# Kernel tuning notes

Measured on AMD Instinct MI355X. Metric: run time of the kernel, lower is better.

## Reference

```python
import jax, jax.numpy as jnp
import numpy as np

HID = 256
DT = 0.05
B = 131072


def setup_inputs() -> dict:
    key = jax.random.key(0)
    ks = jax.random.split(key, 20)
    n = jax.random.normal
    inp = {
        "q": n(ks[0], (B, 1), jnp.float32),
        "p": n(ks[1], (B, 1), jnp.float32),
        "u": n(ks[2], (B, 1), jnp.float32),
        # kinetic MLP T(q_enc, p): in dim 3
        "kW1": n(ks[3], (HID, 3), jnp.float32) / np.sqrt(3.0),
        "kb1": n(ks[4], (HID,), jnp.float32) * 0.01,
        "kW2": n(ks[5], (HID, HID), jnp.float32) / np.sqrt(HID),
        "kb2": n(ks[6], (HID,), jnp.float32) * 0.01,
        "kW3": n(ks[7], (1, HID), jnp.float32) / np.sqrt(HID),
        "kb3": n(ks[8], (1,), jnp.float32) * 0.01,
        # potential MLP V(q_enc): in dim 2
        "pW1": n(ks[9], (HID, 2), jnp.float32) / np.sqrt(2.0),
        "pb1": n(ks[10], (HID,), jnp.float32) * 0.01,
        "pW2": n(ks[11], (HID, HID), jnp.float32) / np.sqrt(HID),
        "pb2": n(ks[12], (HID,), jnp.float32) * 0.01,
        "pW3": n(ks[13], (1, HID), jnp.float32) / np.sqrt(HID),
        "pb3": n(ks[14], (1,), jnp.float32) * 0.01,
        # learned structure matrices (std=0.01 as in nn.init.normal_)
        "A": n(ks[15], (2, 2), jnp.float32) * 0.01,
        "L_param": n(ks[16], (2, 2), jnp.float32) * 0.01,
        "b_ctrl": n(ks[17], (1, 1), jnp.float32) * 0.01,
    }
    return inp


def reference(q, p, u, kW1, kb1, kW2, kb2, kW3, kb3,
              pW1, pb1, pW2, pb2, pW3, pb3, A, L_param, b_ctrl):
    sp = jax.nn.softplus

    def H_sum(z):  # z: [B,2] -> scalar sum of H over batch
        q_, p_ = z[:, :1], z[:, 1:]
        enc = jnp.concatenate([jnp.sin(q_), jnp.cos(q_)], axis=-1)  # [B,2]
        x = jnp.concatenate([enc, p_], axis=-1)                      # [B,3]
        h = sp(x @ kW1.T + kb1)
        h = sp(h @ kW2.T + kb2)
        T = (h @ kW3.T + kb3)[:, 0]
        g = sp(enc @ pW1.T + pb1)
        g = sp(g @ pW2.T + pb2)
        V = (g @ pW3.T + pb3)[:, 0]
        return jnp.sum(T + V)

    # M = J - R with J = A - A^T, R = L L^T, L = strict-lower + softplus(diag)
    J = A - A.T
    L = jnp.tril(L_param, -1) + jnp.diag(sp(jnp.diagonal(L_param)))
    M = J - L @ L.T                          # [2,2]
    Bu = u @ b_ctrl.T                        # [B,1]
    zeros_q = jnp.zeros_like(q)

    def dyn(q_, p_):
        # torch detaches z before autograd.grad -> stop_gradient here
        z = jax.lax.stop_gradient(jnp.concatenate([q_, p_], axis=-1))
        gH = jax.grad(H_sum)(z)              # [B,2] = dH/dz per sample
        dz = gH @ M.T + jnp.concatenate([zeros_q, Bu], axis=-1)
        return dz[:, :1], dz[:, 1:]

    dt = DT
    dq1, dp1 = dyn(q, p)
    dq2, dp2 = dyn(q + 0.5 * dt * dq1, p + 0.5 * dt * dp1)
    dq3, dp3 = dyn(q + 0.5 * dt * dq2, p + 0.5 * dt * dp2)
    dq4, dp4 = dyn(q + dt * dq3, p + dt * dp3)
    q_next = q + dt / 6.0 * (dq1 + 2 * dq2 + 2 * dq3 + dq4)
    p_next = p + dt / 6.0 * (dp1 + 2 * dp2 + 2 * dp3 + dp4)
    return jnp.concatenate([q_next, p_next], axis=-1)  # [B,2]
```

## Files before the change

kernel.cpp:

```cpp
#include <hip/hip_runtime.h>

#define HID 256
#define BT 64
#define DTC 0.05f

typedef __attribute__((ext_vector_type(4))) float f32x4;
typedef __attribute__((ext_vector_type(8))) __bf16 bf16x8;

__device__ __forceinline__ unsigned cvt_pk_bf16(float lo, float hi) {
    unsigned r;
    asm("v_cvt_pk_bf16_f32 %0, %1, %2" : "=v"(r) : "v"(lo), "v"(hi));
    return r;
}

__device__ __forceinline__ unsigned short f2bf(float f) {
    unsigned int x = __float_as_uint(f);
    x += 0x7fffu + ((x >> 16) & 1u);
    return (unsigned short)(x >> 16);
}
__device__ __forceinline__ float bf2f(unsigned short s) {
    return __uint_as_float(((unsigned int)s) << 16);
}

#define OFF_FWDT 0
#define OFF_BWDT 65536
#define OFF_FWDV 131072
#define OFF_BWDV 196608
#define OFF_PROJT 262144
#define OFF_PROJV 266240
#define TOTAL_PRE 270336

__global__ void prepack_kernel(const float* __restrict__ kW1, const float* __restrict__ kW2,
                               const float* __restrict__ pW1, const float* __restrict__ pW2,
                               unsigned short* __restrict__ ws) {
    int t = blockIdx.x * 256 + threadIdx.x;
    if (t >= TOTAL_PRE) return;
    float v;
    if (t < OFF_FWDV) {
        int tt = t & 65535;
        bool bwd = t >= OFF_BWDT;
        int j = tt & 7, lane = (tt >> 3) & 63, kk = (tt >> 9) & 7, nt = tt >> 12;
        int n = nt * 16 + (lane & 15);
        int k = kk * 32 + (lane >> 4) * 8 + j;
        v = bwd ? kW2[k * HID + n] : kW2[n * HID + k];
    } else if (t < OFF_PROJT) {
        int tt = (t - OFF_FWDV) & 65535;
        bool bwd = t >= OFF_BWDV;
        int j = tt & 7, lane = (tt >> 3) & 63, kk = (tt >> 9) & 7, nt = tt >> 12;
        int n = nt * 16 + (lane & 15);
        int k = kk * 32 + (lane >> 4) * 8 + j;
        v = bwd ? pW2[k * HID + n] : pW2[n * HID + k];
    } else if (t < OFF_PROJV) {
        int tt = t - OFF_PROJT;
        int j = tt & 7, lane = (tt >> 3) & 63, kk = tt >> 9;
        int c = lane & 15;
        int k = kk * 32 + (lane >> 4) * 8 + j;
        v = (c < 3) ? kW1[k * 3 + c] : 0.f;
    } else {
        int tt = t - OFF_PROJV;
        int j = tt & 7, lane = (tt >> 3) & 63, kk = tt >> 9;
        int c = lane & 15;
        int k = kk * 32 + (lane >> 4) * 8 + j;
        v = (c < 2) ? pW1[k * 2 + c] : 0.f;
    }
    ws[t] = f2bf(v);
}


#define MFMA __builtin_amdgcn_mfma_f32_16x16x32_bf16

template <int IND, int NOUT>
__device__ __forceinline__ void run_net(
    char* bufAc, char* bufBc,
    const float* sh_sin, const float* sh_cos, const float* sh_pv,
    const float* __restrict__ W1, const float* __restrict__ b1g,
    const float* __restrict__ b2g, const float* __restrict__ W3,
    const unsigned short* __restrict__ fwdB, const unsigned short* __restrict__ bwdB,
    const unsigned short* __restrict__ projB,
    float* g0, float* g1, float* g2,
    int w, int lane)
{
    const int lr = lane & 15;
    const int lg = lane >> 4;
    const unsigned int arx = (unsigned)(lr & 7) << 4;
    const unsigned int cbase = ((unsigned)lg << 4) ^ arx;

    {
        float w0[2], w1v[2], w2v[2], b1v[2];
#pragma unroll
        for (int nt = 0; nt < 2; ++nt) {
            int j = w * 32 + nt * 16 + lr;
            w0[nt]  = W1[j * IND + 0];
            w1v[nt] = W1[j * IND + 1];
            w2v[nt] = (IND == 3) ? W1[j * IND + 2] : 0.f;
            b1v[nt] = b1g[j];
        }
#pragma unroll
        for (int mt = 0; mt < 4; ++mt) {
#pragma unroll
            for (int r = 0; r < 4; ++r) {
                int row = mt * 16 + lg * 4 + r;
                float sv = sh_sin[row], cv = sh_cos[row];
                float pv = (IND == 3) ? sh_pv[row] : 0.f;
                unsigned int rowx = (unsigned)(row & 7) << 4;
                char* rowp = bufAc + row * 512;
                float sp[2];
#pragma unroll
                for (int nt = 0; nt < 2; ++nt) {
                    float x = fmaf(w0[nt], sv, b1v[nt]);
                    x = fmaf(w1v[nt], cv, x);
                    if (IND == 3) x = fmaf(w2v[nt], pv, x);
                    float e = __expf(-fabsf(x));
                    sp[nt] = fmaxf(x, 0.f) + __logf(1.f + e);
                }
                unsigned d01 = cvt_pk_bf16(sp[0], sp[1]);
                int j0 = w * 32 + lr;
                *(unsigned short*)(rowp + (((j0 +  0) * 2) ^ rowx)) = (unsigned short)d01;
                *(unsigned short*)(rowp + (((j0 + 16) * 2) ^ rowx)) = (unsigned short)(d01 >> 16);
            }
        }
    }
    __syncthreads();

    f32x4 acc[4][2];
#pragma unroll
    for (int mt = 0; mt < 4; ++mt)
#pragma unroll
        for (int nt = 0; nt < 2; ++nt)
            acc[mt][nt] = (f32x4){0.f, 0.f, 0.f, 0.f};
    {
        const unsigned short* fb = fwdB + (w * 2) * 8 * 512 + lane * 8;
#pragma unroll 1
        for (int kk = 0; kk < 8; ++kk) {
            bf16x8 bv0 = *(const bf16x8*)(fb + (0 * 8 + kk) * 512);
            bf16x8 bv1 = *(const bf16x8*)(fb + (1 * 8 + kk) * 512);
            unsigned int off = cbase ^ (unsigned)(kk << 6);
#pragma unroll
            for (int mt = 0; mt < 4; ++mt) {
                bf16x8 af = *(const bf16x8*)(bufAc + (mt * 16 + lr) * 512 + off);
                acc[mt][0] = MFMA(af, bv0, acc[mt][0], 0, 0, 0);
                acc[mt][1] = MFMA(af, bv1, acc[mt][1], 0, 0, 0);
            }
        }
    }

    {
        float b2v[2], w3v[2];
#pragma unroll
        for (int nt = 0; nt < 2; ++nt) {
            int j = w * 32 + nt * 16 + lr;
            b2v[nt] = b2g[j];
            w3v[nt] = W3[j];
        }
#pragma unroll
        for (int nt = 0; nt < 2; ++nt) {
            int i = w * 32 + nt * 16 + lr;
#pragma unroll
            for (int mt = 0; mt < 4; ++mt) {
                float val[4];
#pragma unroll
                for (int r = 0; r < 4; ++r) {
                    float x = acc[mt][nt][r] + b2v[nt];
                    float e = __expf(-fabsf(x));
                    float t = __builtin_amdgcn_rcpf(1.f + e);
                    float sg = (x < 0.f) ? e * t : t;
                    val[r] = w3v[nt] * sg;
                }
                unsigned d01 = cvt_pk_bf16(val[0], val[1]);
                unsigned d23 = cvt_pk_bf16(val[2], val[3]);
#pragma unroll
                for (int r = 0; r < 4; ++r) {
                    int row = mt * 16 + lg * 4 + r;
                    unsigned short hv = (r == 0) ? (unsigned short)d01
                                      : (r == 1) ? (unsigned short)(d01 >> 16)
                                      : (r == 2) ? (unsigned short)d23
                                                 : (unsigned short)(d23 >> 16);
                    *(unsigned short*)(bufBc + row * 512 + ((i * 2) ^ ((unsigned)(row & 7) << 4))) = hv;
                }
            }
        }
    }
    __syncthreads();

#pragma unroll
    for (int mt = 0; mt < 4; ++mt)
#pragma unroll
        for (int nt = 0; nt < 2; ++nt)
            acc[mt][nt] = (f32x4){0.f, 0.f, 0.f, 0.f};
    {
        const unsigned short* bb = bwdB + (w * 2) * 8 * 512 + lane * 8;
#pragma unroll 1
        for (int kk = 0; kk < 8; ++kk) {
            bf16x8 bv0 = *(const bf16x8*)(bb + (0 * 8 + kk) * 512);
            bf16x8 bv1 = *(const bf16x8*)(bb + (1 * 8 + kk) * 512);
            unsigned int off = cbase ^ (unsigned)(kk << 6);
#pragma unroll
            for (int mt = 0; mt < 4; ++mt) {
                bf16x8 af = *(const bf16x8*)(bufBc + (mt * 16 + lr) * 512 + off);
                acc[mt][0] = MFMA(af, bv0, acc[mt][0], 0, 0, 0);
                acc[mt][1] = MFMA(af, bv1, acc[mt][1], 0, 0, 0);
            }
        }
    }

#pragma unroll
    for (int mt = 0; mt < 4; ++mt) {
#pragma unroll
        for (int r = 0; r < 4; ++r) {
            int row = mt * 16 + lg * 4 + r;
            unsigned int rowx = (unsigned)(row & 7) << 4;
            char* rowp = bufAc + row * 512;
            int j0 = w * 32 + lr;
            unsigned short* a0 = (unsigned short*)(rowp + (((j0 +  0) * 2) ^ rowx));
            unsigned short* a1 = (unsigned short*)(rowp + (((j0 + 16) * 2) ^ rowx));
            float sg0 = 1.f - __expf(-bf2f(*a0));
            float sg1 = 1.f - __expf(-bf2f(*a1));
            unsigned d01 = cvt_pk_bf16(acc[mt][0][r] * sg0, acc[mt][1][r] * sg1);
            *a0 = (unsigned short)d01;
            *a1 = (unsigned short)(d01 >> 16);
        }
    }
    __syncthreads();

    if (w < 4) {
        const unsigned short* pb = projB + lane * 8;
        f32x4 pacc = (f32x4){0.f, 0.f, 0.f, 0.f};
        char* arow = bufAc + (w * 16 + lr) * 512;
#pragma unroll 1
        for (int kk = 0; kk < 8; ++kk) {
            bf16x8 bv = *(const bf16x8*)(pb + kk * 512);
            bf16x8 af = *(const bf16x8*)(arow + (cbase ^ (unsigned)(kk << 6)));
            pacc = MFMA(af, bv, pacc, 0, 0, 0);
        }
        if (lr < NOUT) {
            float* dst = (lr == 0) ? g0 : ((lr == 1) ? g1 : g2);
#pragma unroll
            for (int r = 0; r < 4; ++r) dst[w * 16 + lg * 4 + r] = pacc[r];
        }
    }
    __syncthreads();
}

__global__ __launch_bounds__(512, 2) void phgn_kernel(
    const float* __restrict__ q, const float* __restrict__ p, const float* __restrict__ u,
    const float* __restrict__ kW1, const float* __restrict__ kb1,
    const float* __restrict__ kb2, const float* __restrict__ kW3,
    const float* __restrict__ pW1, const float* __restrict__ pb1,
    const float* __restrict__ pb2, const float* __restrict__ pW3,
    const float* __restrict__ A, const float* __restrict__ Lp, const float* __restrict__ bctrl,
    const unsigned short* __restrict__ ws, float* __restrict__ out)
{
    __shared__ __attribute__((aligned(16))) unsigned short bufA[BT * HID];
    __shared__ __attribute__((aligned(16))) unsigned short bufB[BT * HID];
    __shared__ float sh_sin[BT], sh_cos[BT], sh_pv[BT];
    __shared__ float gx0[BT], gx1[BT], gx2[BT], ge0[BT], ge1[BT];

    const int tid = threadIdx.x;
    const int w = tid >> 6, lane = tid & 63;
    const int base = blockIdx.x * BT;

    float l00 = __logf(1.f + __expf(Lp[0]));
    float l11 = __logf(1.f + __expf(Lp[3]));
    float l10 = Lp[2];
    float J01 = A[1] - A[2];
    float M00 = -(l00 * l00);
    float M01 = J01 - l00 * l10;
    float M10 = -J01 - l10 * l00;
    float M11 = -(l10 * l10 + l11 * l11);

    float q0 = 0.f, p0 = 0.f, buv = 0.f, aq = 0.f, ap = 0.f;
    if (tid < BT) {
        q0 = q[base + tid]; p0 = p[base + tid]; buv = u[base + tid] * bctrl[0];
        float s, c; __sincosf(q0, &s, &c);
        sh_sin[tid] = s; sh_cos[tid] = c; sh_pv[tid] = p0;
    }
    __syncthreads();

    char* bufAc = (char*)bufA;
    char* bufBc = (char*)bufB;
#pragma unroll 1
    for (int s = 0; s < 4; ++s) {
        run_net<3, 3>(bufAc, bufBc, sh_sin, sh_cos, sh_pv, kW1, kb1, kb2, kW3,
                      ws + OFF_FWDT, ws + OFF_BWDT, ws + OFF_PROJT, gx0, gx1, gx2, w, lane);
        run_net<2, 2>(bufAc, bufBc, sh_sin, sh_cos, sh_pv, pW1, pb1, pb2, pW3,
                      ws + OFF_FWDV, ws + OFF_BWDV, ws + OFF_PROJV, ge0, ge1, ge1, w, lane);
        if (tid < BT) {
            float gq = (gx0[tid] + ge0[tid]) * sh_cos[tid] - (gx1[tid] + ge1[tid]) * sh_sin[tid];
            float gp = gx2[tid];
            float dq = M00 * gq + M01 * gp;
            float dp = M10 * gq + M11 * gp + buv;
            float wgt = (s == 0 || s == 3) ? 1.f : 2.f;
            aq += wgt * dq; ap += wgt * dp;
            if (s < 3) {
                float cs = (s == 2) ? 1.f : 0.5f;
                float qs = fmaf(cs * DTC, dq, q0);
                float ps = fmaf(cs * DTC, dp, p0);
                float sn, cn; __sincosf(qs, &sn, &cn);
                sh_sin[tid] = sn; sh_cos[tid] = cn; sh_pv[tid] = ps;
            } else {
                float qn = fmaf(DTC / 6.f, aq, q0);
                float pn = fmaf(DTC / 6.f, ap, p0);
                ((float2*)out)[base + tid] = make_float2(qn, pn);
            }
        }
        __syncthreads();
    }
}

extern "C" void kernel_launch(void* const* d_in, const int* in_sizes, int n_in,
                              void* d_out, int out_size, void* d_ws, size_t ws_size,
                              hipStream_t stream) {
    const float* q    = (const float*)d_in[0];
    const float* p    = (const float*)d_in[1];
    const float* u    = (const float*)d_in[2];
    const float* kW1  = (const float*)d_in[3];
    const float* kb1  = (const float*)d_in[4];
    const float* kW2  = (const float*)d_in[5];
    const float* kb2  = (const float*)d_in[6];
    const float* kW3  = (const float*)d_in[7];
    const float* pW1  = (const float*)d_in[9];
    const float* pb1  = (const float*)d_in[10];
    const float* pW2  = (const float*)d_in[11];
    const float* pb2  = (const float*)d_in[12];
    const float* pW3  = (const float*)d_in[13];
    const float* A    = (const float*)d_in[15];
    const float* Lp   = (const float*)d_in[16];
    const float* bctl = (const float*)d_in[17];
    unsigned short* ws = (unsigned short*)d_ws;
    float* out = (float*)d_out;
    int B = in_sizes[0];

    prepack_kernel<<<(TOTAL_PRE + 255) / 256, 256, 0, stream>>>(kW1, kW2, pW1, pW2, ws);
    phgn_kernel<<<B / BT, 512, 0, stream>>>(q, p, u, kW1, kb1, kb2, kW3,
                                            pW1, pb1, pb2, pW3, A, Lp, bctl, ws, out);
}
```

Before: 756.3 us.

## Hoist per-thread weights, prefetch B fragments, keep layer-1 sigmoid in registers

Per-thread first-layer weights, biases and output weights for both MLPs are loaded once per kernel into registers instead of on every RK stage. Global B-fragment loads are software-pipelined one k-step ahead, and the first fragments are issued before the barrier to hide latency. The layer-1 sigmoid derivative is computed exactly at forward time and kept packed in registers as bf16, replacing the LDS reread and exp-based reconstruction in the backward pass. The M coefficients are made wave-uniform via readfirstlane. These changes raise register pressure, which could hurt occupancy under the 512x2 launch bounds.

```diff
diff --git a/kernel.cpp b/kernel.cpp
--- a/kernel.cpp
+++ b/kernel.cpp
@@ -18,8 +18,9 @@
     x += 0x7fffu + ((x >> 16) & 1u);
     return (unsigned short)(x >> 16);
 }
-__device__ __forceinline__ float bf2f(unsigned short s) {
-    return __uint_as_float(((unsigned int)s) << 16);
+
+__device__ __forceinline__ float sgpr_f(float v) {
+    return __uint_as_float(__builtin_amdgcn_readfirstlane(__float_as_uint(v)));
 }
 
 #define OFF_FWDT 0
@@ -69,12 +70,13 @@
 
 #define MFMA __builtin_amdgcn_mfma_f32_16x16x32_bf16
 
+struct NetRegs { float w0[2], w1[2], w2[2], b1[2], b2[2], w3[2]; };
+
 template <int IND, int NOUT>
 __device__ __forceinline__ void run_net(
     char* bufAc, char* bufBc,
     const float* sh_sin, const float* sh_cos, const float* sh_pv,
-    const float* __restrict__ W1, const float* __restrict__ b1g,
-    const float* __restrict__ b2g, const float* __restrict__ W3,
+    const NetRegs& R,
     const unsigned short* __restrict__ fwdB, const unsigned short* __restrict__ bwdB,
     const unsigned short* __restrict__ projB,
     float* g0, float* g1, float* g2,
@@ -85,41 +87,39 @@
     const unsigned int arx = (unsigned)(lr & 7) << 4;
     const unsigned int cbase = ((unsigned)lg << 4) ^ arx;
 
-    {
-        float w0[2], w1v[2], w2v[2], b1v[2];
-#pragma unroll
-        for (int nt = 0; nt < 2; ++nt) {
-            int j = w * 32 + nt * 16 + lr;
-            w0[nt]  = W1[j * IND + 0];
-            w1v[nt] = W1[j * IND + 1];
-            w2v[nt] = (IND == 3) ? W1[j * IND + 2] : 0.f;
-            b1v[nt] = b1g[j];
-        }
-#pragma unroll
-        for (int mt = 0; mt < 4; ++mt) {
-#pragma unroll
-            for (int r = 0; r < 4; ++r) {
-                int row = mt * 16 + lg * 4 + r;
-                float sv = sh_sin[row], cv = sh_cos[row];
-                float pv = (IND == 3) ? sh_pv[row] : 0.f;
-                unsigned int rowx = (unsigned)(row & 7) << 4;
-                char* rowp = bufAc + row * 512;
-                float sp[2];
-#pragma unroll
-                for (int nt = 0; nt < 2; ++nt) {
-                    float x = fmaf(w0[nt], sv, b1v[nt]);
-                    x = fmaf(w1v[nt], cv, x);
-                    if (IND == 3) x = fmaf(w2v[nt], pv, x);
-                    float e = __expf(-fabsf(x));
-                    sp[nt] = fmaxf(x, 0.f) + __logf(1.f + e);
-                }
-                unsigned d01 = cvt_pk_bf16(sp[0], sp[1]);
-                int j0 = w * 32 + lr;
-                *(unsigned short*)(rowp + (((j0 +  0) * 2) ^ rowx)) = (unsigned short)d01;
-                *(unsigned short*)(rowp + (((j0 + 16) * 2) ^ rowx)) = (unsigned short)(d01 >> 16);
-            }
-        }
-    }
+    unsigned s1p[16];
+
+#pragma unroll
+    for (int mt = 0; mt < 4; ++mt) {
+#pragma unroll
+        for (int r = 0; r < 4; ++r) {
+            int row = mt * 16 + lg * 4 + r;
+            float sv = sh_sin[row], cv = sh_cos[row];
+            float pv = (IND == 3) ? sh_pv[row] : 0.f;
+            unsigned int rowx = (unsigned)(row & 7) << 4;
+            char* rowp = bufAc + row * 512;
+            float sp[2], sg[2];
+#pragma unroll
+            for (int nt = 0; nt < 2; ++nt) {
+                float x = fmaf(R.w0[nt], sv, R.b1[nt]);
+                x = fmaf(R.w1[nt], cv, x);
+                if (IND == 3) x = fmaf(R.w2[nt], pv, x);
+                float e = __expf(-fabsf(x));
+                sp[nt] = fmaxf(x, 0.f) + __logf(1.f + e);
+                float t = __builtin_amdgcn_rcpf(1.f + e);
+                sg[nt] = (x < 0.f) ? e * t : t;
+            }
+            unsigned d01 = cvt_pk_bf16(sp[0], sp[1]);
+            int j0 = w * 32 + lr;
+            *(unsigned short*)(rowp + (((j0 +  0) * 2) ^ rowx)) = (unsigned short)d01;
+            *(unsigned short*)(rowp + (((j0 + 16) * 2) ^ rowx)) = (unsigned short)(d01 >> 16);
+            s1p[mt * 4 + r] = cvt_pk_bf16(sg[0], sg[1]);
+        }
+    }
+
+    const unsigned short* fb = fwdB + (w * 2) * 8 * 512 + lane * 8;
+    bf16x8 c0 = *(const bf16x8*)(fb + 0 * 512);
+    bf16x8 c1 = *(const bf16x8*)(fb + 8 * 512);
     __syncthreads();
 
     f32x4 acc[4][2];
@@ -129,57 +129,59 @@
         for (int nt = 0; nt < 2; ++nt)
             acc[mt][nt] = (f32x4){0.f, 0.f, 0.f, 0.f};
     {
-        const unsigned short* fb = fwdB + (w * 2) * 8 * 512 + lane * 8;
 #pragma unroll 1
         for (int kk = 0; kk < 8; ++kk) {
-            bf16x8 bv0 = *(const bf16x8*)(fb + (0 * 8 + kk) * 512);
-            bf16x8 bv1 = *(const bf16x8*)(fb + (1 * 8 + kk) * 512);
             unsigned int off = cbase ^ (unsigned)(kk << 6);
-#pragma unroll
-            for (int mt = 0; mt < 4; ++mt) {
-                bf16x8 af = *(const bf16x8*)(bufAc + (mt * 16 + lr) * 512 + off);
-                acc[mt][0] = MFMA(af, bv0, acc[mt][0], 0, 0, 0);
-                acc[mt][1] = MFMA(af, bv1, acc[mt][1], 0, 0, 0);
-            }
-        }
-    }
-
-    {
-        float b2v[2], w3v[2];
-#pragma unroll
-        for (int nt = 0; nt < 2; ++nt) {
-            int j = w * 32 + nt * 16 + lr;
-            b2v[nt] = b2g[j];
-            w3v[nt] = W3[j];
-        }
-#pragma unroll
-        for (int nt = 0; nt < 2; ++nt) {
-            int i = w * 32 + nt * 16 + lr;
-#pragma unroll
-            for (int mt = 0; mt < 4; ++mt) {
-                float val[4];
-#pragma unroll
-                for (int r = 0; r < 4; ++r) {
-                    float x = acc[mt][nt][r] + b2v[nt];
-                    float e = __expf(-fabsf(x));
-                    float t = __builtin_amdgcn_rcpf(1.f + e);
-                    float sg = (x < 0.f) ? e * t : t;
-                    val[r] = w3v[nt] * sg;
-                }
-                unsigned d01 = cvt_pk_bf16(val[0], val[1]);
-                unsigned d23 = cvt_pk_bf16(val[2], val[3]);
-#pragma unroll
-                for (int r = 0; r < 4; ++r) {
-                    int row = mt * 16 + lg * 4 + r;
-                    unsigned short hv = (r == 0) ? (unsigned short)d01
-                                      : (r == 1) ? (unsigned short)(d01 >> 16)
-                                      : (r == 2) ? (unsigned short)d23
-                                                 : (unsigned short)(d23 >> 16);
-                    *(unsigned short*)(bufBc + row * 512 + ((i * 2) ^ ((unsigned)(row & 7) << 4))) = hv;
-                }
-            }
-        }
-    }
+            bf16x8 af0 = *(const bf16x8*)(bufAc + (0 * 16 + lr) * 512 + off);
+            bf16x8 af1 = *(const bf16x8*)(bufAc + (1 * 16 + lr) * 512 + off);
+            bf16x8 af2 = *(const bf16x8*)(bufAc + (2 * 16 + lr) * 512 + off);
+            bf16x8 af3 = *(const bf16x8*)(bufAc + (3 * 16 + lr) * 512 + off);
+            acc[0][0] = MFMA(af0, c0, acc[0][0], 0, 0, 0);
+            acc[0][1] = MFMA(af0, c1, acc[0][1], 0, 0, 0);
+            acc[1][0] = MFMA(af1, c0, acc[1][0], 0, 0, 0);
+            acc[1][1] = MFMA(af1, c1, acc[1][1], 0, 0, 0);
+            acc[2][0] = MFMA(af2, c0, acc[2][0], 0, 0, 0);
+            acc[2][1] = MFMA(af2, c1, acc[2][1], 0, 0, 0);
+            acc[3][0] = MFMA(af3, c0, acc[3][0], 0, 0, 0);
+            acc[3][1] = MFMA(af3, c1, acc[3][1], 0, 0, 0);
+            if (kk < 7) {
+                c0 = *(const bf16x8*)(fb + (0 * 8 + kk + 1) * 512);
+                c1 = *(const bf16x8*)(fb + (1 * 8 + kk + 1) * 512);
+            }
+        }
+    }
+
+#pragma unroll
+    for (int nt = 0; nt < 2; ++nt) {
+        int i = w * 32 + nt * 16 + lr;
+#pragma unroll
+        for (int mt = 0; mt < 4; ++mt) {
+            float val[4];
+#pragma unroll
+            for (int r = 0; r < 4; ++r) {
+                float x = acc[mt][nt][r] + R.b2[nt];
+                float e = __expf(-fabsf(x));
+                float t = __builtin_amdgcn_rcpf(1.f + e);
+                float sg = (x < 0.f) ? e * t : t;
+                val[r] = R.w3[nt] * sg;
+            }
+            unsigned d01 = cvt_pk_bf16(val[0], val[1]);
+            unsigned d23 = cvt_pk_bf16(val[2], val[3]);
+#pragma unroll
+            for (int r = 0; r < 4; ++r) {
+                int row = mt * 16 + lg * 4 + r;
+                unsigned short hv = (r == 0) ? (unsigned short)d01
+                                  : (r == 1) ? (unsigned short)(d01 >> 16)
+                                  : (r == 2) ? (unsigned short)d23
+                                             : (unsigned short)(d23 >> 16);
+                *(unsigned short*)(bufBc + row * 512 + ((i * 2) ^ ((unsigned)(row & 7) << 4))) = hv;
+            }
+        }
+    }
+
+    const unsigned short* bb = bwdB + (w * 2) * 8 * 512 + lane * 8;
+    c0 = *(const bf16x8*)(bb + 0 * 512);
+    c1 = *(const bf16x8*)(bb + 8 * 512);
     __syncthreads();
 
 #pragma unroll
@@ -188,17 +190,24 @@
         for (int nt = 0; nt < 2; ++nt)
             acc[mt][nt] = (f32x4){0.f, 0.f, 0.f, 0.f};
     {
-        const unsigned short* bb = bwdB + (w * 2) * 8 * 512 + lane * 8;
 #pragma unroll 1
         for (int kk = 0; kk < 8; ++kk) {
-            bf16x8 bv0 = *(const bf16x8*)(bb + (0 * 8 + kk) * 512);
-            bf16x8 bv1 = *(const bf16x8*)(bb + (1 * 8 + kk) * 512);
             unsigned int off = cbase ^ (unsigned)(kk << 6);
-#pragma unroll
-            for (int mt = 0; mt < 4; ++mt) {
-                bf16x8 af = *(const bf16x8*)(bufBc + (mt * 16 + lr) * 512 + off);
-                acc[mt][0] = MFMA(af, bv0, acc[mt][0], 0, 0, 0);
-                acc[mt][1] = MFMA(af, bv1, acc[mt][1], 0, 0, 0);
+            bf16x8 af0 = *(const bf16x8*)(bufBc + (0 * 16 + lr) * 512 + off);
+            bf16x8 af1 = *(const bf16x8*)(bufBc + (1 * 16 + lr) * 512 + off);
+            bf16x8 af2 = *(const bf16x8*)(bufBc + (2 * 16 + lr) * 512 + off);
+            bf16x8 af3 = *(const bf16x8*)(bufBc + (3 * 16 + lr) * 512 + off);
+            acc[0][0] = MFMA(af0, c0, acc[0][0], 0, 0, 0);
+            acc[0][1] = MFMA(af0, c1, acc[0][1], 0, 0, 0);
+            acc[1][0] = MFMA(af1, c0, acc[1][0], 0, 0, 0);
+            acc[1][1] = MFMA(af1, c1, acc[1][1], 0, 0, 0);
+            acc[2][0] = MFMA(af2, c0, acc[2][0], 0, 0, 0);
+            acc[2][1] = MFMA(af2, c1, acc[2][1], 0, 0, 0);
+            acc[3][0] = MFMA(af3, c0, acc[3][0], 0, 0, 0);
+            acc[3][1] = MFMA(af3, c1, acc[3][1], 0, 0, 0);
+            if (kk < 7) {
+                c0 = *(const bf16x8*)(bb + (0 * 8 + kk + 1) * 512);
+                c1 = *(const bf16x8*)(bb + (1 * 8 + kk + 1) * 512);
             }
         }
     }
@@ -210,14 +219,13 @@
             int row = mt * 16 + lg * 4 + r;
             unsigned int rowx = (unsigned)(row & 7) << 4;
             char* rowp = bufAc + row * 512;
+            unsigned pa = s1p[mt * 4 + r];
+            float sg0 = __uint_as_float(pa << 16);
+            float sg1 = __uint_as_float(pa & 0xffff0000u);
+            unsigned d01 = cvt_pk_bf16(acc[mt][0][r] * sg0, acc[mt][1][r] * sg1);
             int j0 = w * 32 + lr;
-            unsigned short* a0 = (unsigned short*)(rowp + (((j0 +  0) * 2) ^ rowx));
-            unsigned short* a1 = (unsigned short*)(rowp + (((j0 + 16) * 2) ^ rowx));
-            float sg0 = 1.f - __expf(-bf2f(*a0));
-            float sg1 = 1.f - __expf(-bf2f(*a1));
-            unsigned d01 = cvt_pk_bf16(acc[mt][0][r] * sg0, acc[mt][1][r] * sg1);
-            *a0 = (unsigned short)d01;
-            *a1 = (unsigned short)(d01 >> 16);
+            *(unsigned short*)(rowp + (((j0 +  0) * 2) ^ rowx)) = (unsigned short)d01;
+            *(unsigned short*)(rowp + (((j0 + 16) * 2) ^ rowx)) = (unsigned short)(d01 >> 16);
         }
     }
     __syncthreads();
@@ -257,16 +265,35 @@
 
     const int tid = threadIdx.x;
     const int w = tid >> 6, lane = tid & 63;
+    const int lr = lane & 15;
     const int base = blockIdx.x * BT;
+
+    NetRegs RT, RV;
+#pragma unroll
+    for (int nt = 0; nt < 2; ++nt) {
+        int j = w * 32 + nt * 16 + lr;
+        RT.w0[nt] = kW1[j * 3 + 0];
+        RT.w1[nt] = kW1[j * 3 + 1];
+        RT.w2[nt] = kW1[j * 3 + 2];
+        RT.b1[nt] = kb1[j];
+        RT.b2[nt] = kb2[j];
+        RT.w3[nt] = kW3[j];
+        RV.w0[nt] = pW1[j * 2 + 0];
+        RV.w1[nt] = pW1[j * 2 + 1];
+        RV.w2[nt] = 0.f;
+        RV.b1[nt] = pb1[j];
+        RV.b2[nt] = pb2[j];
+        RV.w3[nt] = pW3[j];
+    }
 
     float l00 = __logf(1.f + __expf(Lp[0]));
     float l11 = __logf(1.f + __expf(Lp[3]));
     float l10 = Lp[2];
     float J01 = A[1] - A[2];
-    float M00 = -(l00 * l00);
-    float M01 = J01 - l00 * l10;
-    float M10 = -J01 - l10 * l00;
-    float M11 = -(l10 * l10 + l11 * l11);
+    float M00 = sgpr_f(-(l00 * l00));
+    float M01 = sgpr_f(J01 - l00 * l10);
+    float M10 = sgpr_f(-J01 - l10 * l00);
+    float M11 = sgpr_f(-(l10 * l10 + l11 * l11));
 
     float q0 = 0.f, p0 = 0.f, buv = 0.f, aq = 0.f, ap = 0.f;
     if (tid < BT) {
@@ -280,9 +307,9 @@
     char* bufBc = (char*)bufB;
 #pragma unroll 1
     for (int s = 0; s < 4; ++s) {
-        run_net<3, 3>(bufAc, bufBc, sh_sin, sh_cos, sh_pv, kW1, kb1, kb2, kW3,
+        run_net<3, 3>(bufAc, bufBc, sh_sin, sh_cos, sh_pv, RT,
                       ws + OFF_FWDT, ws + OFF_BWDT, ws + OFF_PROJT, gx0, gx1, gx2, w, lane);
-        run_net<2, 2>(bufAc, bufBc, sh_sin, sh_cos, sh_pv, pW1, pb1, pb2, pW3,
+        run_net<2, 2>(bufAc, bufBc, sh_sin, sh_cos, sh_pv, RV,
                       ws + OFF_FWDV, ws + OFF_BWDV, ws + OFF_PROJV, ge0, ge1, ge1, w, lane);
         if (tid < BT) {
             float gq = (gx0[tid] + ge0[tid]) * sh_cos[tid] - (gx1[tid] + ge1[tid]) * sh_sin[tid];
```

Result: faster. 715.2 us (-5.4%).
